# Kernel tuning notes

Measured on AMD Instinct MI355X. Metric: run time of the kernel, lower is better.

## Reference

```python
import jax, jax.numpy as jnp
import numpy as np

N, IN_DIM, HID, OUT_DIM, E, L = 100000, 128, 128, 64, 1600000, 4
ALPHA = 0.6


def gcn_conv(x, W, b, src, dst, deg_inv_sqrt):
    # PyG GCNConv: add self-loops, symmetric norm, linear, scatter-add, bias
    xw = x @ W                                    # [N, H]
    norm = deg_inv_sqrt[src] * deg_inv_sqrt[dst]  # [E]
    msg = xw[src] * norm[:, None]                 # [E, H] (memory-bound gather)
    agg = jax.ops.segment_sum(msg, dst, num_segments=N)
    # self-loop contribution: weight 1 * deg^-1
    agg = agg + xw * (deg_inv_sqrt * deg_inv_sqrt)[:, None]
    return agg + b


def setup_inputs() -> dict:
    key = jax.random.key(0)
    ks = jax.random.split(key, 8)
    s = 1.0 / np.sqrt(HID)
    x = jax.random.normal(ks[0], (N, IN_DIM), dtype=jnp.float32)
    edge_index = jax.random.randint(ks[1], (2, E), 0, N, dtype=jnp.int64)
    W1 = jax.random.uniform(ks[2], (IN_DIM, HID), jnp.float32, -s, s)
    b1 = jnp.zeros((HID,), jnp.float32)
    convW = jax.random.uniform(ks[3], (L, HID, HID), jnp.float32, -s, s)
    convB = jnp.zeros((L, HID), jnp.float32)
    W2 = jax.random.uniform(ks[4], (HID, OUT_DIM), jnp.float32, -s, s)
    b2 = jnp.zeros((OUT_DIM,), jnp.float32)
    return {"x": x, "edge_index": edge_index, "W1": W1, "b1": b1,
            "convW": convW, "convB": convB, "W2": W2, "b2": b2}


def reference(x, edge_index, W1, b1, convW, convB, W2, b2):
    src, dst = edge_index[0], edge_index[1]
    # degree with self-loops (gcn_norm with edge weight 1 on dst/col)
    deg = jax.ops.segment_sum(jnp.ones((E,), x.dtype), dst, num_segments=N) + 1.0
    deg_inv_sqrt = 1.0 / jnp.sqrt(deg)

    Z = x @ W1 + b1
    z_init = Z
    z_sum = jnp.zeros_like(Z)
    for i in range(L):
        Z = jax.nn.relu(gcn_conv(Z, convW[i], convB[i], src, dst, deg_inv_sqrt))
        z_sum = z_sum + Z
    out = ALPHA * z_init + (1.0 - ALPHA) * z_sum / L
    return out @ W2 + b2
```

## Files before the change

### kernel.cpp

```cpp
#include <hip/hip_runtime.h>

#define HID 128
#define NLAYERS 4

typedef __attribute__((ext_vector_type(8))) short bf16x8;
typedef __attribute__((ext_vector_type(8))) unsigned short u16x8;
typedef __attribute__((ext_vector_type(4))) float f32x4;

static __device__ __forceinline__ float bf2f(unsigned short u) {
    return __uint_as_float(((unsigned)u) << 16);
}
static __device__ __forceinline__ unsigned short f2bf(float f) {
    unsigned u = __float_as_uint(f);
    return (unsigned short)((u + 0x7FFF + ((u >> 16) & 1)) >> 16);
}


__global__ void zero_i32(int* p, int n) {
    int i = blockIdx.x * blockDim.x + threadIdx.x;
    if (i < n) p[i] = 0;
}

__global__ void hist_kernel(const int* __restrict__ dst, int* __restrict__ cnt, int E) {
    int e = blockIdx.x * blockDim.x + threadIdx.x;
    if (e < E) atomicAdd(&cnt[dst[e]], 1);
}

__global__ void dis_kernel(const int* __restrict__ cnt, float* __restrict__ dis, int n) {
    int i = blockIdx.x * blockDim.x + threadIdx.x;
    if (i < n) dis[i] = rsqrtf((float)cnt[i] + 1.0f);
}

__global__ void scan1(const int* __restrict__ cnt, int* __restrict__ rowp,
                      int* __restrict__ bsums, int n) {
    __shared__ int s[1024];
    int tid = threadIdx.x;
    int gid = blockIdx.x * 1024 + tid;
    int v = (gid < n) ? cnt[gid] : 0;
    s[tid] = v;
    __syncthreads();
    for (int off = 1; off < 1024; off <<= 1) {
        int t = (tid >= off) ? s[tid - off] : 0;
        __syncthreads();
        s[tid] += t;
        __syncthreads();
    }
    if (gid < n) rowp[gid] = s[tid] - v;
    if (tid == 1023) bsums[blockIdx.x] = s[1023];
}

__global__ void scan2(int* bsums, int nb) {
    if (threadIdx.x == 0 && blockIdx.x == 0) {
        int run = 0;
        for (int i = 0; i < nb; ++i) { int t = bsums[i]; bsums[i] = run; run += t; }
    }
}

__global__ void scan3(int* __restrict__ rowp, const int* __restrict__ bsums, int n, int E) {
    int gid = blockIdx.x * 1024 + threadIdx.x;
    if (gid < n) rowp[gid] += bsums[blockIdx.x];
    if (gid == 0) rowp[n] = E;
}

__global__ void scatter_kernel(const int* __restrict__ src, const int* __restrict__ dst,
                               const int* __restrict__ rowp, int* __restrict__ cursor,
                               const float* __restrict__ dis, int2* __restrict__ csr, int E) {
    int e = blockIdx.x * blockDim.x + threadIdx.x;
    if (e < E) {
        int d = dst[e], s = src[e];
        int pos = rowp[d] + atomicAdd(&cursor[d], 1);
        int2 v;
        v.x = s;
        v.y = __float_as_int(dis[s]);
        csr[pos] = v;
    }
}


__global__ void wprep(const float* __restrict__ W1, const float* __restrict__ convW,
                      const float* __restrict__ W2, unsigned short* __restrict__ W1t,
                      unsigned short* __restrict__ convWt, unsigned short* __restrict__ W2t) {
    int r = blockIdx.x;
    int k = threadIdx.x;
    const float* src;
    unsigned short* dst;
    int ncols, n;
    if (r < 128) { src = W1; dst = W1t; n = r; ncols = 128; }
    else if (r < 640) {
        int l = (r - 128) >> 7; n = (r - 128) & 127;
        src = convW + (size_t)l * 16384; dst = convWt + (size_t)l * 16384; ncols = 128;
    } else { src = W2; dst = W2t; n = r - 640; ncols = 64; }
    dst[(size_t)n * 128 + k] = f2bf(src[(size_t)k * ncols + n]);
}

__global__ void xcast(const float* __restrict__ x, unsigned short* __restrict__ xb, int n8) {
    int i = blockIdx.x * blockDim.x + threadIdx.x;
    if (i >= n8) return;
    float4 v0 = *(const float4*)&x[(size_t)i * 8];
    float4 v1 = *(const float4*)&x[(size_t)i * 8 + 4];
    u16x8 o;
    o[0] = f2bf(v0.x); o[1] = f2bf(v0.y); o[2] = f2bf(v0.z); o[3] = f2bf(v0.w);
    o[4] = f2bf(v1.x); o[5] = f2bf(v1.y); o[6] = f2bf(v1.z); o[7] = f2bf(v1.w);
    *(u16x8*)&xb[(size_t)i * 8] = o;
}


template <bool BIAS>
__global__ __launch_bounds__(256, 2) void gemm128_mfma(
    const unsigned short* __restrict__ A, const unsigned short* __restrict__ Bt,
    const float* __restrict__ bias, unsigned short* __restrict__ C, int nrows) {
    int wid = threadIdx.x >> 6, lane = threadIdx.x & 63;
    int l15 = lane & 15, l4 = lane >> 4;

    bf16x8 b[8][4];
#pragma unroll
    for (int nt = 0; nt < 8; ++nt)
#pragma unroll
        for (int ks = 0; ks < 4; ++ks)
            b[nt][ks] = *(const bf16x8*)&Bt[(size_t)(nt * 16 + l15) * 128 + ks * 32 + l4 * 8];
    float bb[8];
    if (BIAS) {
#pragma unroll
        for (int nt = 0; nt < 8; ++nt) bb[nt] = bias[nt * 16 + l15];
    }

    for (int s2 = 0; s2 < 2; ++s2) {
        int row0 = (blockIdx.x * 8 + wid * 2 + s2) * 16;
        if (row0 >= nrows) break;
        int ar = min(row0 + l15, nrows - 1);
        bf16x8 a[4];
#pragma unroll
        for (int ks = 0; ks < 4; ++ks)
            a[ks] = *(const bf16x8*)&A[(size_t)ar * 128 + ks * 32 + l4 * 8];
        f32x4 acc[8] = {};
#pragma unroll
        for (int ks = 0; ks < 4; ++ks)
#pragma unroll
            for (int nt = 0; nt < 8; ++nt)
                acc[nt] = __builtin_amdgcn_mfma_f32_16x16x32_bf16(a[ks], b[nt][ks], acc[nt], 0, 0, 0);
#pragma unroll
        for (int nt = 0; nt < 8; ++nt) {
            int col = nt * 16 + l15;
#pragma unroll
            for (int r = 0; r < 4; ++r) {
                int row = row0 + l4 * 4 + r;
                if (row < nrows) {
                    float v = acc[nt][r];
                    if (BIAS) v += bb[nt];
                    C[(size_t)row * 128 + col] = f2bf(v);
                }
            }
        }
    }
}


__global__ __launch_bounds__(256, 2) void gemm_final(
    const unsigned short* __restrict__ z0, const unsigned short* __restrict__ z1,
    const unsigned short* __restrict__ z2, const unsigned short* __restrict__ z3,
    const unsigned short* __restrict__ z4, const unsigned short* __restrict__ Bt,
    const float* __restrict__ bias, float* __restrict__ out, int nrows) {
    int wid = threadIdx.x >> 6, lane = threadIdx.x & 63;
    int l15 = lane & 15, l4 = lane >> 4;

    bf16x8 b[4][4];
#pragma unroll
    for (int nt = 0; nt < 4; ++nt)
#pragma unroll
        for (int ks = 0; ks < 4; ++ks)
            b[nt][ks] = *(const bf16x8*)&Bt[(size_t)(nt * 16 + l15) * 128 + ks * 32 + l4 * 8];
    float bb[4];
#pragma unroll
    for (int nt = 0; nt < 4; ++nt) bb[nt] = bias[nt * 16 + l15];

    const unsigned short* zs[5] = { z0, z1, z2, z3, z4 };

    for (int s2 = 0; s2 < 2; ++s2) {
        int row0 = (blockIdx.x * 8 + wid * 2 + s2) * 16;
        if (row0 >= nrows) break;
        int ar = min(row0 + l15, nrows - 1);
        bf16x8 a[5][4];
#pragma unroll
        for (int st = 0; st < 5; ++st)
#pragma unroll
            for (int ks = 0; ks < 4; ++ks)
                a[st][ks] = *(const bf16x8*)&zs[st][(size_t)ar * 128 + ks * 32 + l4 * 8];
        f32x4 acc0[4] = {};
        f32x4 acc1[4] = {};
#pragma unroll
        for (int st = 0; st < 5; ++st)
#pragma unroll
            for (int ks = 0; ks < 4; ++ks)
#pragma unroll
                for (int nt = 0; nt < 4; ++nt) {
                    if (st == 0)
                        acc0[nt] = __builtin_amdgcn_mfma_f32_16x16x32_bf16(a[0][ks], b[nt][ks], acc0[nt], 0, 0, 0);
                    else
                        acc1[nt] = __builtin_amdgcn_mfma_f32_16x16x32_bf16(a[st][ks], b[nt][ks], acc1[nt], 0, 0, 0);
                }
#pragma unroll
        for (int nt = 0; nt < 4; ++nt) {
            int col = nt * 16 + l15;
#pragma unroll
            for (int r = 0; r < 4; ++r) {
                int row = row0 + l4 * 4 + r;
                if (row < nrows)
                    out[(size_t)row * 64 + col] = 0.6f * acc0[nt][r] + 0.1f * acc1[nt][r] + bb[nt];
            }
        }
    }
}


__global__ __launch_bounds__(256) void spmm_kernel(
    const unsigned short* __restrict__ xwb, const int* __restrict__ rowp,
    const int2* __restrict__ csr, const float* __restrict__ dis,
    const float* __restrict__ bias, unsigned short* __restrict__ Z, int n) {
    int l = threadIdx.x & 15;
    int node = blockIdx.x * 16 + (threadIdx.x >> 4);
    if (node >= n) return;
    const u16x8* xw8 = (const u16x8*)xwb;

    float acc[8] = {};
    int beg = rowp[node], end = rowp[node + 1];
    int e = beg;
    for (; e + 1 < end; e += 2) {
        int2 s0 = csr[e];
        int2 s1 = csr[e + 1];
        u16x8 x0 = xw8[(size_t)s0.x * 16 + l];
        u16x8 x1 = xw8[(size_t)s1.x * 16 + l];
        float w0 = __int_as_float(s0.y);
        float w1 = __int_as_float(s1.y);
#pragma unroll
        for (int j = 0; j < 8; ++j) acc[j] = fmaf(w0, bf2f(x0[j]), acc[j]);
#pragma unroll
        for (int j = 0; j < 8; ++j) acc[j] = fmaf(w1, bf2f(x1[j]), acc[j]);
    }
    if (e < end) {
        int2 s0 = csr[e];
        u16x8 x0 = xw8[(size_t)s0.x * 16 + l];
        float w0 = __int_as_float(s0.y);
#pragma unroll
        for (int j = 0; j < 8; ++j) acc[j] = fmaf(w0, bf2f(x0[j]), acc[j]);
    }

    float d = dis[node];
    float d2 = d * d;
    u16x8 xs = xw8[(size_t)node * 16 + l];
    float4 b0 = *(const float4*)&bias[l * 8];
    float4 b1 = *(const float4*)&bias[l * 8 + 4];
    float bbv[8] = { b0.x, b0.y, b0.z, b0.w, b1.x, b1.y, b1.z, b1.w };
    u16x8 ov;
#pragma unroll
    for (int j = 0; j < 8; ++j)
        ov[j] = f2bf(fmaxf(fmaf(d, acc[j], fmaf(d2, bf2f(xs[j]), bbv[j])), 0.f));
    *(u16x8*)&Z[(size_t)node * HID + l * 8] = ov;
}


extern "C" void kernel_launch(void* const* d_in, const int* in_sizes, int n_in,
                              void* d_out, int out_size, void* d_ws, size_t ws_size,
                              hipStream_t stream) {
    const float* x     = (const float*)d_in[0];
    const int*   ei    = (const int*)d_in[1];
    const float* W1    = (const float*)d_in[2];
    const float* b1    = (const float*)d_in[3];
    const float* convW = (const float*)d_in[4];
    const float* convB = (const float*)d_in[5];
    const float* W2    = (const float*)d_in[6];
    const float* b2    = (const float*)d_in[7];

    const int N = in_sizes[0] / HID;
    const int E = in_sizes[1] / 2;
    const int* src = ei;
    const int* dst = ei + E;

    char* p = (char*)d_ws;
    auto alloc = [&](size_t bytes) {
        void* q = (void*)p;
        p += (bytes + 255) & ~(size_t)255;
        return q;
    };
    float* dis   = (float*)alloc((size_t)N * 4);
    int*   cnt   = (int*)alloc((size_t)N * 4);
    int*   rowp  = (int*)alloc((size_t)(N + 1) * 4);
    int*   bsums = (int*)alloc(4096);
    int2*  csr   = (int2*)alloc((size_t)E * 8);
    unsigned short* xb  = (unsigned short*)alloc((size_t)N * HID * 2);
    unsigned short* xw  = (unsigned short*)alloc((size_t)N * HID * 2);
    unsigned short* Zs[5];
    for (int i = 0; i < 4; ++i) Zs[i] = (unsigned short*)alloc((size_t)N * HID * 2);
    Zs[4] = xb;
    unsigned short* W1t    = (unsigned short*)alloc(128 * 128 * 2);
    unsigned short* convWt = (unsigned short*)alloc((size_t)NLAYERS * 128 * 128 * 2);
    unsigned short* W2t    = (unsigned short*)alloc(64 * 128 * 2);

    const int nb = (N + 1023) / 1024;
    const int gemmBlocks = (N + 127) / 128;

    wprep<<<704, 128, 0, stream>>>(W1, convW, W2, W1t, convWt, W2t);
    xcast<<<(N * 16 + 255) / 256, 256, 0, stream>>>(x, xb, N * 16);

    zero_i32<<<(N + 255) / 256, 256, 0, stream>>>(cnt, N);
    hist_kernel<<<(E + 255) / 256, 256, 0, stream>>>(dst, cnt, E);
    dis_kernel<<<(N + 255) / 256, 256, 0, stream>>>(cnt, dis, N);
    scan1<<<nb, 1024, 0, stream>>>(cnt, rowp, bsums, N);
    scan2<<<1, 64, 0, stream>>>(bsums, nb);
    scan3<<<nb, 1024, 0, stream>>>(rowp, bsums, N, E);
    zero_i32<<<(N + 255) / 256, 256, 0, stream>>>(cnt, N);
    scatter_kernel<<<(E + 255) / 256, 256, 0, stream>>>(src, dst, rowp, cnt, dis, csr, E);

    gemm128_mfma<true><<<gemmBlocks, 256, 0, stream>>>(xb, W1t, b1, Zs[0], N);

    for (int l = 0; l < NLAYERS; ++l) {
        gemm128_mfma<false><<<gemmBlocks, 256, 0, stream>>>(
            Zs[l], convWt + (size_t)l * 16384, nullptr, xw, N);
        spmm_kernel<<<(N + 15) / 16, 256, 0, stream>>>(
            xw, rowp, csr, dis, convB + (size_t)l * HID, Zs[l + 1], N);
    }

    gemm_final<<<gemmBlocks, 256, 0, stream>>>(
        Zs[0], Zs[1], Zs[2], Zs[3], Zs[4], W2t, b2, (float*)d_out, N);
}
```

Measured before the change: 705.4 us.

## Build CSR via two-level bucketed counting sort and unroll SpMM by four

Replaces the global-atomic histogram, three-kernel scan and atomic scatter with a two-level counting sort. Edges are first binned into 64-node buckets using per-chunk shared-memory histograms, then sorted within each bucket in shared memory. The full symmetric norm is folded into each edge weight, so the SpMM no longer multiplies by the destination's dis. The SpMM inner loop is unrolled to four edges to raise memory-level parallelism. The packed 20-bit source encoding assumes N fits in 2^20, and MAXBUCK assumes at most 1600 buckets.

Measured after the change: 666.7 us. 5.5% less time.

```diff
diff --git a/kernel.cpp b/kernel.cpp
--- a/kernel.cpp
+++ b/kernel.cpp
@@ -2,6 +2,8 @@
 
 #define HID 128
 #define NLAYERS 4
+#define MAXBUCK 1600
+#define CHUNK 16384
 
 typedef __attribute__((ext_vector_type(8))) short bf16x8;
 typedef __attribute__((ext_vector_type(8))) unsigned short u16x8;
@@ -16,63 +18,126 @@
 }
 
 
-__global__ void zero_i32(int* p, int n) {
-    int i = blockIdx.x * blockDim.x + threadIdx.x;
-    if (i < n) p[i] = 0;
-}
-
-__global__ void hist_kernel(const int* __restrict__ dst, int* __restrict__ cnt, int E) {
-    int e = blockIdx.x * blockDim.x + threadIdx.x;
-    if (e < E) atomicAdd(&cnt[dst[e]], 1);
-}
-
-__global__ void dis_kernel(const int* __restrict__ cnt, float* __restrict__ dis, int n) {
-    int i = blockIdx.x * blockDim.x + threadIdx.x;
-    if (i < n) dis[i] = rsqrtf((float)cnt[i] + 1.0f);
-}
-
-__global__ void scan1(const int* __restrict__ cnt, int* __restrict__ rowp,
-                      int* __restrict__ bsums, int n) {
-    __shared__ int s[1024];
+__global__ __launch_bounds__(256) void bin1(const int* __restrict__ dst,
+                                            int* __restrict__ cnt2d, int E, int nbuck) {
+    __shared__ int h[MAXBUCK];
     int tid = threadIdx.x;
-    int gid = blockIdx.x * 1024 + tid;
-    int v = (gid < n) ? cnt[gid] : 0;
-    s[tid] = v;
-    __syncthreads();
-    for (int off = 1; off < 1024; off <<= 1) {
-        int t = (tid >= off) ? s[tid - off] : 0;
+    for (int i = tid; i < nbuck; i += 256) h[i] = 0;
+    __syncthreads();
+    int e0 = blockIdx.x * CHUNK;
+    int e1 = min(e0 + CHUNK, E);
+    for (int e = e0 + tid; e < e1; e += 256) atomicAdd(&h[dst[e] >> 6], 1);
+    __syncthreads();
+    for (int i = tid; i < nbuck; i += 256)
+        cnt2d[(size_t)blockIdx.x * nbuck + i] = h[i];
+}
+
+__global__ void colscan(int* __restrict__ cnt2d, int* __restrict__ colsum,
+                        int nchunks, int nbuck) {
+    int b = blockIdx.x * blockDim.x + threadIdx.x;
+    if (b >= nbuck) return;
+    int run = 0;
+    for (int c = 0; c < nchunks; ++c) {
+        size_t idx = (size_t)c * nbuck + b;
+        int v = cnt2d[idx];
+        cnt2d[idx] = run;
+        run += v;
+    }
+    colsum[b] = run;
+}
+
+__global__ __launch_bounds__(256) void basescan(const int* __restrict__ colsum,
+                                                int* __restrict__ base, int nbuck) {
+    __shared__ int part[256];
+    int tid = threadIdx.x;
+    const int per = 7;
+    int loc[per];
+    int run = 0;
+    for (int i = 0; i < per; ++i) {
+        int idx = tid * per + i;
+        int v = (idx < nbuck) ? colsum[idx] : 0;
+        run += v;
+        loc[i] = run;
+    }
+    part[tid] = run;
+    __syncthreads();
+    for (int off = 1; off < 256; off <<= 1) {
+        int t = (tid >= off) ? part[tid - off] : 0;
         __syncthreads();
-        s[tid] += t;
+        part[tid] += t;
         __syncthreads();
     }
-    if (gid < n) rowp[gid] = s[tid] - v;
-    if (tid == 1023) bsums[blockIdx.x] = s[1023];
-}
-
-__global__ void scan2(int* bsums, int nb) {
-    if (threadIdx.x == 0 && blockIdx.x == 0) {
+    int prev = tid ? part[tid - 1] : 0;
+    if (tid == 0) base[0] = 0;
+    for (int i = 0; i < per; ++i) {
+        int idx = tid * per + i;
+        if (idx < nbuck) base[idx + 1] = prev + loc[i];
+    }
+}
+
+__global__ __launch_bounds__(256) void bin2(const int* __restrict__ src, const int* __restrict__ dst,
+                                            const int* __restrict__ cnt2d, const int* __restrict__ base,
+                                            unsigned* __restrict__ ecoarse, int E, int nbuck) {
+    __shared__ int cur[MAXBUCK];
+    int tid = threadIdx.x;
+    for (int i = tid; i < nbuck; i += 256)
+        cur[i] = base[i] + cnt2d[(size_t)blockIdx.x * nbuck + i];
+    __syncthreads();
+    int e0 = blockIdx.x * CHUNK;
+    int e1 = min(e0 + CHUNK, E);
+    for (int e = e0 + tid; e < e1; e += 256) {
+        int d = dst[e];
+        int b = d >> 6;
+        int pos = atomicAdd(&cur[b], 1);
+        ecoarse[pos] = (unsigned)src[e] | ((unsigned)(d & 63) << 20);
+    }
+}
+
+__global__ __launch_bounds__(64) void degdis(const unsigned* __restrict__ ecoarse,
+                                             const int* __restrict__ base,
+                                             float* __restrict__ dis, int N) {
+    __shared__ int cnt[64];
+    int b = blockIdx.x, t = threadIdx.x;
+    cnt[t] = 0;
+    __syncthreads();
+    int s = base[b], e = base[b + 1];
+    for (int i = s + t; i < e; i += 64) atomicAdd(&cnt[ecoarse[i] >> 20], 1);
+    __syncthreads();
+    int node = b * 64 + t;
+    if (node < N) dis[node] = rsqrtf((float)cnt[t] + 1.0f);
+}
+
+__global__ __launch_bounds__(256) void finesort(const unsigned* __restrict__ ecoarse,
+                                                const int* __restrict__ base,
+                                                const float* __restrict__ dis,
+                                                int2* __restrict__ csr, int* __restrict__ rowp,
+                                                int N, int E) {
+    __shared__ int h[64], off[64];
+    int b = blockIdx.x, tid = threadIdx.x;
+    if (tid < 64) h[tid] = 0;
+    __syncthreads();
+    int s = base[b], e = base[b + 1];
+    for (int i = s + tid; i < e; i += 256) atomicAdd(&h[ecoarse[i] >> 20], 1);
+    __syncthreads();
+    if (tid == 0) {
         int run = 0;
-        for (int i = 0; i < nb; ++i) { int t = bsums[i]; bsums[i] = run; run += t; }
-    }
-}
-
-__global__ void scan3(int* __restrict__ rowp, const int* __restrict__ bsums, int n, int E) {
-    int gid = blockIdx.x * 1024 + threadIdx.x;
-    if (gid < n) rowp[gid] += bsums[blockIdx.x];
-    if (gid == 0) rowp[n] = E;
-}
-
-__global__ void scatter_kernel(const int* __restrict__ src, const int* __restrict__ dst,
-                               const int* __restrict__ rowp, int* __restrict__ cursor,
-                               const float* __restrict__ dis, int2* __restrict__ csr, int E) {
-    int e = blockIdx.x * blockDim.x + threadIdx.x;
-    if (e < E) {
-        int d = dst[e], s = src[e];
-        int pos = rowp[d] + atomicAdd(&cursor[d], 1);
-        int2 v;
-        v.x = s;
-        v.y = __float_as_int(dis[s]);
-        csr[pos] = v;
+        for (int i = 0; i < 64; ++i) { off[i] = run; run += h[i]; }
+    }
+    __syncthreads();
+    int node = b * 64 + tid;
+    if (tid < 64 && node < N) rowp[node] = s + off[tid];
+    if (b == 0 && tid == 0) rowp[N] = E;
+    if (tid < 64) h[tid] = off[tid];
+    __syncthreads();
+    for (int i = s + tid; i < e; i += 256) {
+        unsigned v = ecoarse[i];
+        int srcn = v & 0xFFFFF;
+        int dl = v >> 20;
+        int pos = atomicAdd(&h[dl], 1);
+        int2 o;
+        o.x = srcn;
+        o.y = __float_as_int(dis[srcn] * dis[b * 64 + dl]);
+        csr[s + pos] = o;
     }
 }
 
@@ -224,19 +289,28 @@
     float acc[8] = {};
     int beg = rowp[node], end = rowp[node + 1];
     int e = beg;
-    for (; e + 1 < end; e += 2) {
+    for (; e + 4 <= end; e += 4) {
         int2 s0 = csr[e];
         int2 s1 = csr[e + 1];
+        int2 s2 = csr[e + 2];
+        int2 s3 = csr[e + 3];
         u16x8 x0 = xw8[(size_t)s0.x * 16 + l];
         u16x8 x1 = xw8[(size_t)s1.x * 16 + l];
+        u16x8 x2 = xw8[(size_t)s2.x * 16 + l];
+        u16x8 x3 = xw8[(size_t)s3.x * 16 + l];
         float w0 = __int_as_float(s0.y);
         float w1 = __int_as_float(s1.y);
-#pragma unroll
-        for (int j = 0; j < 8; ++j) acc[j] = fmaf(w0, bf2f(x0[j]), acc[j]);
-#pragma unroll
-        for (int j = 0; j < 8; ++j) acc[j] = fmaf(w1, bf2f(x1[j]), acc[j]);
-    }
-    if (e < end) {
+        float w2 = __int_as_float(s2.y);
+        float w3 = __int_as_float(s3.y);
+#pragma unroll
+        for (int j = 0; j < 8; ++j) {
+            acc[j] = fmaf(w0, bf2f(x0[j]), acc[j]);
+            acc[j] = fmaf(w1, bf2f(x1[j]), acc[j]);
+            acc[j] = fmaf(w2, bf2f(x2[j]), acc[j]);
+            acc[j] = fmaf(w3, bf2f(x3[j]), acc[j]);
+        }
+    }
+    for (; e < end; ++e) {
         int2 s0 = csr[e];
         u16x8 x0 = xw8[(size_t)s0.x * 16 + l];
         float w0 = __int_as_float(s0.y);
@@ -253,7 +327,7 @@
     u16x8 ov;
 #pragma unroll
     for (int j = 0; j < 8; ++j)
-        ov[j] = f2bf(fmaxf(fmaf(d, acc[j], fmaf(d2, bf2f(xs[j]), bbv[j])), 0.f));
+        ov[j] = f2bf(fmaxf(acc[j] + fmaf(d2, bf2f(xs[j]), bbv[j]), 0.f));
     *(u16x8*)&Z[(size_t)node * HID + l * 8] = ov;
 }
 
@@ -274,6 +348,8 @@
     const int E = in_sizes[1] / 2;
     const int* src = ei;
     const int* dst = ei + E;
+    const int nbuck = (N + 63) / 64;
+    const int nchunks = (E + CHUNK - 1) / CHUNK;
 
     char* p = (char*)d_ws;
     auto alloc = [&](size_t bytes) {
@@ -281,13 +357,15 @@
         p += (bytes + 255) & ~(size_t)255;
         return q;
     };
-    float* dis   = (float*)alloc((size_t)N * 4);
-    int*   cnt   = (int*)alloc((size_t)N * 4);
-    int*   rowp  = (int*)alloc((size_t)(N + 1) * 4);
-    int*   bsums = (int*)alloc(4096);
-    int2*  csr   = (int2*)alloc((size_t)E * 8);
-    unsigned short* xb  = (unsigned short*)alloc((size_t)N * HID * 2);
-    unsigned short* xw  = (unsigned short*)alloc((size_t)N * HID * 2);
+    float* dis      = (float*)alloc((size_t)N * 4);
+    int*   rowp     = (int*)alloc((size_t)(N + 1) * 4);
+    int*   base     = (int*)alloc((size_t)(nbuck + 1) * 4);
+    int*   colsum   = (int*)alloc((size_t)nbuck * 4);
+    int*   cnt2d    = (int*)alloc((size_t)nchunks * nbuck * 4);
+    unsigned* ecoarse = (unsigned*)alloc((size_t)E * 4);
+    int2*  csr      = (int2*)alloc((size_t)E * 8);
+    unsigned short* xb = (unsigned short*)alloc((size_t)N * HID * 2);
+    unsigned short* xw = (unsigned short*)alloc((size_t)N * HID * 2);
     unsigned short* Zs[5];
     for (int i = 0; i < 4; ++i) Zs[i] = (unsigned short*)alloc((size_t)N * HID * 2);
     Zs[4] = xb;
@@ -295,20 +373,17 @@
     unsigned short* convWt = (unsigned short*)alloc((size_t)NLAYERS * 128 * 128 * 2);
     unsigned short* W2t    = (unsigned short*)alloc(64 * 128 * 2);
 
-    const int nb = (N + 1023) / 1024;
     const int gemmBlocks = (N + 127) / 128;
 
     wprep<<<704, 128, 0, stream>>>(W1, convW, W2, W1t, convWt, W2t);
     xcast<<<(N * 16 + 255) / 256, 256, 0, stream>>>(x, xb, N * 16);
 
-    zero_i32<<<(N + 255) / 256, 256, 0, stream>>>(cnt, N);
-    hist_kernel<<<(E + 255) / 256, 256, 0, stream>>>(dst, cnt, E);
-    dis_kernel<<<(N + 255) / 256, 256, 0, stream>>>(cnt, dis, N);
-    scan1<<<nb, 1024, 0, stream>>>(cnt, rowp, bsums, N);
-    scan2<<<1, 64, 0, stream>>>(bsums, nb);
-    scan3<<<nb, 1024, 0, stream>>>(rowp, bsums, N, E);
-    zero_i32<<<(N + 255) / 256, 256, 0, stream>>>(cnt, N);
-    scatter_kernel<<<(E + 255) / 256, 256, 0, stream>>>(src, dst, rowp, cnt, dis, csr, E);
+    bin1<<<nchunks, 256, 0, stream>>>(dst, cnt2d, E, nbuck);
+    colscan<<<(nbuck + 255) / 256, 256, 0, stream>>>(cnt2d, colsum, nchunks, nbuck);
+    basescan<<<1, 256, 0, stream>>>(colsum, base, nbuck);
+    bin2<<<nchunks, 256, 0, stream>>>(src, dst, cnt2d, base, ecoarse, E, nbuck);
+    degdis<<<nbuck, 64, 0, stream>>>(ecoarse, base, dis, N);
+    finesort<<<nbuck, 256, 0, stream>>>(ecoarse, base, dis, csr, rowp, N, E);
 
     gemm128_mfma<true><<<gemmBlocks, 256, 0, stream>>>(xb, W1t, b1, Zs[0], N);
 
```
